# Kernel tuning notes

Hardware: AMD Instinct MI355X
Metric: run time of the kernel (lower is better)

## Reference

```python
import jax, jax.numpy as jnp
import numpy as np

NUM_EMBED = 1024
NUM_HEADS = 16
BLOCK_SIZE = 2048


def setup_inputs() -> dict:
    key = jax.random.key(0)
    k1, k2, k3, k4, k5 = jax.random.split(key, 5)
    C = NUM_EMBED
    s = 1.0 / np.sqrt(C)
    x = jax.random.normal(k1, (2, BLOCK_SIZE, C), dtype=jnp.float32)
    # nn.Linear params: weight (out,in), bias (out,)
    w_attn = jax.random.uniform(k2, (3 * C, C), minval=-s, maxval=s, dtype=jnp.float32)
    b_attn = jax.random.uniform(k3, (3 * C,), minval=-s, maxval=s, dtype=jnp.float32)
    w_proj = jax.random.uniform(k4, (C, C), minval=-s, maxval=s, dtype=jnp.float32)
    b_proj = jax.random.uniform(k5, (C,), minval=-s, maxval=s, dtype=jnp.float32)
    return {"x": x, "w_attn": w_attn, "b_attn": b_attn, "w_proj": w_proj, "b_proj": b_proj}


def reference(x, w_attn, b_attn, w_proj, b_proj):
    B, T, C = x.shape
    H = NUM_HEADS
    D = C // H
    kqv = jnp.einsum('btc,oc->bto', x, w_attn) + b_attn  # (B,T,3C)
    # Original code splits as K, Q, V in that order.
    K, Q, V = jnp.split(kqv, 3, axis=2)
    K = K.reshape(B, T, H, D).transpose(0, 2, 1, 3)  # (B,H,T,D)
    Q = Q.reshape(B, T, H, D).transpose(0, 2, 1, 3)
    V = V.reshape(B, T, H, D).transpose(0, 2, 1, 3)
    aff = jnp.einsum('bhqd,bhkd->bhqk', Q, K) * (D ** -0.5)  # (B,H,T,T)
    causal = jnp.tril(jnp.ones((T, T), dtype=bool))
    aff = jnp.where(causal[None, None], aff, jnp.float32(-jnp.inf))
    wei = jax.nn.softmax(aff, axis=-1)
    attn = jnp.einsum('bhqk,bhkd->bhqd', wei, V)
    attn = attn.transpose(0, 2, 1, 3).reshape(B, T, C)
    out = jnp.einsum('btc,oc->bto', attn, w_proj) + b_proj
    return out
```

## Files before the change

### kernel.cpp

```cpp
#include <hip/hip_runtime.h>
#include <hip/hip_bf16.h>
#include <cstdint>

typedef __attribute__((ext_vector_type(8))) short bf16x8;
typedef __attribute__((ext_vector_type(4))) float f32x4;
typedef __attribute__((ext_vector_type(16))) float f32x16;
typedef __attribute__((ext_vector_type(4))) uint16_t u16x4;

__device__ __forceinline__ uint16_t f2b(float f) {
  union { float f; uint32_t i; } v; v.f = f;
  return (uint16_t)((v.i + 0x7FFFu + ((v.i >> 16) & 1u)) >> 16);
}

__device__ __forceinline__ uint32_t pkbf(float a, float b) {
  union { __hip_bfloat162 h2; uint32_t u; } c;
  c.h2 = __float22bfloat162_rn(make_float2(a, b));
  return c.u;
}

#define GLDS16(g, l) __builtin_amdgcn_global_load_lds( \
    (const __attribute__((address_space(1))) void*)(g), \
    (__attribute__((address_space(3))) void*)(l), 16, 0, 0)

__global__ __launch_bounds__(256) void cvt_all(
    const float* __restrict__ x, const float* __restrict__ wa, const float* __restrict__ wp,
    uint16_t* __restrict__ xb, uint16_t* __restrict__ wab, uint16_t* __restrict__ wpb) {
  const int i = (blockIdx.x * 256 + threadIdx.x) * 4;
  const float* src; uint16_t* dst; int off;
  if (i < 4194304)      { src = x;  dst = xb;  off = i; }
  else if (i < 7340032) { src = wa; dst = wab; off = i - 4194304; }
  else                  { src = wp; dst = wpb; off = i - 7340032; }
  const float4 v = *(const float4*)(src + off);
  u16x4 o;
  o.x = f2b(v.x); o.y = f2b(v.y); o.z = f2b(v.z); o.w = f2b(v.w);
  *(u16x4*)(dst + off) = o;
}

template <int BM, bool OUT_BF16>
__global__ __launch_bounds__(256) void gemm_bt_bias(
    const uint16_t* __restrict__ A, const uint16_t* __restrict__ B,
    const float* __restrict__ bias, void* __restrict__ Cv,
    int M, int N, int K) {
  constexpr int MI = BM / 32;
  constexpr int CA = BM / 16;
  constexpr int CPW = (2 * (CA + 8)) / 4;
  constexpr int CT_PITCH = OUT_BF16 ? 72 : 68;
  constexpr size_t CT_BYTES = (size_t)4 * (BM / 2) * CT_PITCH * (OUT_BF16 ? 2 : 4);
  constexpr size_t ST_BYTES = (size_t)(2 * (BM * 32 + 4096)) * 2;
  constexpr size_t LB = CT_BYTES > ST_BYTES ? CT_BYTES : ST_BYTES;
  __shared__ alignas(16) unsigned char ldsb[LB];
  uint16_t* lds = (uint16_t*)ldsb;
  const int offB0 = BM * 32;
  const int offA1 = BM * 32 + 4096;
  const int offB1 = 2 * BM * 32 + 4096;

  const int tid = threadIdx.x;
  const int wave = tid >> 6, lane = tid & 63;
  const int q4 = lane >> 4, l16 = lane & 15;
  const int wm = wave >> 1, wn = wave & 1;
  const long blockM = (long)blockIdx.y * BM;
  const long blockN = (long)blockIdx.x * 128;

  f32x4 acc[MI][4] = {};

  for (int k0 = 0; k0 < K; k0 += 64) {
#pragma unroll
    for (int c = 0; c < CPW; ++c) {
      const int id = c * 4 + wave;
      const uint16_t* mat; long rowBase; int a, kk, off;
      if (id < CA)               { mat = A; rowBase = blockM; a = id;            kk = k0;      off = 0; }
      else if (id < CA + 8)      { mat = B; rowBase = blockN; a = id - CA;       kk = k0;      off = offB0; }
      else if (id < 2 * CA + 8)  { mat = A; rowBase = blockM; a = id - CA - 8;   kk = k0 + 32; off = offA1; }
      else                       { mat = B; rowBase = blockN; a = id - 2*CA - 8; kk = k0 + 32; off = offB1; }
      const int flat = a * 64 + lane;
      const int row = flat >> 2, seg = flat & 3;
      GLDS16(mat + (rowBase + row) * (long)K + kk + seg * 8, lds + off + a * 512);
    }
    __syncthreads();
#pragma unroll
    for (int h = 0; h < 2; ++h) {
      const uint16_t* Ah = lds + (h ? offA1 : 0);
      const uint16_t* Bh = lds + (h ? offB1 : offB0);
      bf16x8 af[MI], bfr[4];
#pragma unroll
      for (int i = 0; i < MI; ++i)
        af[i] = *(const bf16x8*)&Ah[(wm * (BM / 2) + i * 16 + l16) * 32 + q4 * 8];
#pragma unroll
      for (int j = 0; j < 4; ++j)
        bfr[j] = *(const bf16x8*)&Bh[(wn * 64 + j * 16 + l16) * 32 + q4 * 8];
#pragma unroll
      for (int i = 0; i < MI; ++i)
#pragma unroll
        for (int j = 0; j < 4; ++j)
          acc[i][j] = __builtin_amdgcn_mfma_f32_16x16x32_bf16(af[i], bfr[j], acc[i][j], 0, 0, 0);
    }
    __syncthreads();
  }

  if (OUT_BF16) {
    uint16_t* ct = lds + wave * (BM / 2) * 72;
#pragma unroll
    for (int j = 0; j < 4; ++j) {
      const float bv = bias[blockN + wn * 64 + j * 16 + l16];
#pragma unroll
      for (int i = 0; i < MI; ++i)
#pragma unroll
        for (int r = 0; r < 4; ++r)
          ct[(i * 16 + q4 * 4 + r) * 72 + j * 16 + l16] = f2b(acc[i][j][r] + bv);
    }
    __syncthreads();
    uint16_t* Cb = (uint16_t*)Cv;
#pragma unroll
    for (int st = 0; st < BM / 16; ++st) {
      const int flat = st * 64 + lane;
      const int row = flat >> 3, seg = flat & 7;
      const bf16x8 v = *(const bf16x8*)&ct[row * 72 + seg * 8];
      *(bf16x8*)&Cb[(blockM + wm * (BM / 2) + row) * (long)N + blockN + wn * 64 + seg * 8] = v;
    }
  } else {
    float* ct = (float*)ldsb + wave * (BM / 2) * 68;
#pragma unroll
    for (int j = 0; j < 4; ++j) {
      const float bv = bias[blockN + wn * 64 + j * 16 + l16];
#pragma unroll
      for (int i = 0; i < MI; ++i)
#pragma unroll
        for (int r = 0; r < 4; ++r)
          ct[(i * 16 + q4 * 4 + r) * 68 + j * 16 + l16] = acc[i][j][r] + bv;
    }
    __syncthreads();
    float* Cb = (float*)Cv;
#pragma unroll
    for (int st = 0; st < BM / 8; ++st) {
      const int flat = st * 64 + lane;
      const int row = flat >> 4, seg = flat & 15;
      const f32x4 v = *(const f32x4*)&ct[row * 68 + seg * 4];
      *(f32x4*)&Cb[(blockM + wm * (BM / 2) + row) * (long)N + blockN + wn * 64 + seg * 4] = v;
    }
  }
}

__global__ __launch_bounds__(256, 2) void attn_flash(
    const uint16_t* __restrict__ kqv, uint16_t* __restrict__ attn) {
  constexpr int T = 2048, C = 1024, C3 = 3072;
  __shared__ uint16_t KP[128 * 72];
  __shared__ uint16_t Vt[64 * 136];
  uint32_t* VtW = (uint32_t*)Vt;

  const int tid = threadIdx.x;
  const int wave = tid >> 6, lane = tid & 63;
  const int l32 = lane & 31, hh = lane >> 5;
  const int sidx = blockIdx.x >> 5, bh = blockIdx.x & 31;
  const int b = bh >> 4, h = bh & 15;
  const size_t base = (size_t)b * T * C3;
  const int hD = h * 64;

  const int tr = tid >> 3, kch = tid & 7;
  const float sc = 0.125f * 1.4426950408889634f;

  const int qb = (sidx < 8) ? (15 - sidx) : (sidx - 8);
  const int nkt = qb + 1;
  const int qrow = qb * 128 + wave * 32 + l32;

  bf16x8 qf[4];
#pragma unroll
  for (int m = 0; m < 4; ++m)
    qf[m] = *(const bf16x8*)&kqv[base + (size_t)qrow * C3 + C + hD + m * 16 + hh * 8];

  f32x16 o[2] = {};
  float m_i = -1e30f, l_i = 0.f;

  bf16x8 pk[4], pv0[2], pv1[2];
#pragma unroll
  for (int rr = 0; rr < 4; ++rr)
    pk[rr] = *(const bf16x8*)&kqv[base + (size_t)(rr * 32 + tr) * C3 + hD + kch * 8];
#pragma unroll
  for (int s2 = 0; s2 < 2; ++s2) {
    const size_t g = base + (size_t)(2 * (s2 * 32 + tr)) * C3 + 2 * C + hD + kch * 8;
    pv0[s2] = *(const bf16x8*)&kqv[g];
    pv1[s2] = *(const bf16x8*)&kqv[g + C3];
  }

  for (int kt = 0; kt < nkt; ++kt) {
    __syncthreads();
#pragma unroll
    for (int rr = 0; rr < 4; ++rr)
      *(bf16x8*)&KP[(rr * 32 + tr) * 72 + kch * 8] = pk[rr];
#pragma unroll
    for (int s2 = 0; s2 < 2; ++s2) {
      const int colw = ((s2 * 32 + tr) + 8 * kch) & 63;
      const uint32_t* a0 = (const uint32_t*)&pv0[s2];
      const uint32_t* a1 = (const uint32_t*)&pv1[s2];
#pragma unroll
      for (int i = 0; i < 8; ++i) {
        const uint32_t w = (i & 1)
            ? __builtin_amdgcn_perm(a1[i >> 1], a0[i >> 1], 0x07060302u)
            : __builtin_amdgcn_perm(a1[i >> 1], a0[i >> 1], 0x05040100u);
        VtW[(kch * 8 + i) * 68 + colw] = w;
      }
    }
    __syncthreads();
    if (kt + 1 < nkt) {
      const int kb2 = (kt + 1) * 128;
#pragma unroll
      for (int rr = 0; rr < 4; ++rr)
        pk[rr] = *(const bf16x8*)&kqv[base + (size_t)(kb2 + rr * 32 + tr) * C3 + hD + kch * 8];
#pragma unroll
      for (int s2 = 0; s2 < 2; ++s2) {
        const size_t g = base + (size_t)(kb2 + 2 * (s2 * 32 + tr)) * C3 + 2 * C + hD + kch * 8;
        pv0[s2] = *(const bf16x8*)&kqv[g];
        pv1[s2] = *(const bf16x8*)&kqv[g + C3];
      }
    }

    const int kbmax = (kt == qb) ? wave : 3;

    f32x16 z[4];
#pragma unroll
    for (int kb = 0; kb < 4; ++kb) {
      if (kb <= kbmax) {
        f32x16 zz = {};
#pragma unroll
        for (int m = 0; m < 4; ++m) {
          const bf16x8 kf = *(const bf16x8*)&KP[(kb * 32 + l32) * 72 + m * 16 + hh * 8];
          zz = __builtin_amdgcn_mfma_f32_32x32x16_bf16(kf, qf[m], zz, 0, 0, 0);
        }
        if (kt == qb && kb == wave) {
#pragma unroll
          for (int r = 0; r < 16; ++r) {
            const int keyl = (r & 3) + 8 * (r >> 2) + 4 * hh;
            if (keyl > l32) zz[r] = -1e30f;
          }
        }
        z[kb] = zz;
      }
    }

    float mloc = -1e30f;
#pragma unroll
    for (int kb = 0; kb < 4; ++kb)
      if (kb <= kbmax)
#pragma unroll
        for (int r = 0; r < 16; ++r) mloc = fmaxf(mloc, z[kb][r]);
    mloc = fmaxf(mloc, __shfl_xor(mloc, 32, 64));
    const float mnew = fmaxf(m_i, mloc * sc);
    const float alpha = exp2f(m_i - mnew);
    const bool mchg = mnew > m_i;
    m_i = mnew;
    float rs = 0.f;
#pragma unroll
    for (int kb = 0; kb < 4; ++kb)
      if (kb <= kbmax)
#pragma unroll
        for (int r = 0; r < 16; ++r) {
          const float pe = exp2f(fmaf(z[kb][r], sc, -mnew));
          z[kb][r] = pe;
          rs += pe;
        }
    rs += __shfl_xor(rs, 32, 64);
    l_i = l_i * alpha + rs;
    if (__any(mchg)) {
#pragma unroll
      for (int r = 0; r < 16; ++r) {
        const float ar = __shfl(alpha, (r & 3) + 8 * (r >> 2) + 4 * hh, 64);
        o[0][r] *= ar;
        o[1][r] *= ar;
      }
    }

#pragma unroll
    for (int kb = 0; kb < 4; ++kb) {
      if (kb <= kbmax) {
        uint32_t x0 = pkbf(z[kb][0], z[kb][1]),   x1 = pkbf(z[kb][2], z[kb][3]);
        uint32_t y0 = pkbf(z[kb][4], z[kb][5]),   y1 = pkbf(z[kb][6], z[kb][7]);
        uint32_t x2 = pkbf(z[kb][8], z[kb][9]),   x3 = pkbf(z[kb][10], z[kb][11]);
        uint32_t y2 = pkbf(z[kb][12], z[kb][13]), y3 = pkbf(z[kb][14], z[kb][15]);
        const uint32_t s0 = hh ? x0 : y0, s1 = hh ? x1 : y1;
        const uint32_t s2 = hh ? x2 : y2, s3 = hh ? x3 : y3;
        const uint32_t t0 = __shfl_xor(s0, 32, 64), t1 = __shfl_xor(s1, 32, 64);
        const uint32_t t2 = __shfl_xor(s2, 32, 64), t3 = __shfl_xor(s3, 32, 64);
#pragma unroll
        for (int cc = 0; cc < 2; ++cc) {
          const int c = 2 * kb + cc;
          union { bf16x8 v; uint32_t w[4]; } pa;
          if (cc == 0) {
            pa.w[0] = hh ? t0 : x0; pa.w[1] = hh ? t1 : x1;
            pa.w[2] = hh ? y0 : t0; pa.w[3] = hh ? y1 : t1;
          } else {
            pa.w[0] = hh ? t2 : x2; pa.w[1] = hh ? t3 : x3;
            pa.w[2] = hh ? y2 : t2; pa.w[3] = hh ? y3 : t3;
          }
#pragma unroll
          for (int db = 0; db < 2; ++db) {
            const int d = db * 32 + l32;
            const int col = (c * 16 + hh * 8 + 16 * (d >> 3)) & 127;
            const bf16x8 vf = *(const bf16x8*)&Vt[d * 136 + col];
            o[db] = __builtin_amdgcn_mfma_f32_32x32x16_bf16(pa.v, vf, o[db], 0, 0, 0);
          }
        }
      }
    }
  }

  const size_t obase = (size_t)b * T * C;
  const float linv = 1.0f / l_i;
#pragma unroll
  for (int r = 0; r < 16; ++r) {
    const int ql = (r & 3) + 8 * (r >> 2) + 4 * hh;
    const float lr = __shfl(linv, ql, 64);
    const int q = qb * 128 + wave * 32 + ql;
    const size_t rowoff = obase + (size_t)q * C + hD;
    attn[rowoff + l32] = f2b(o[0][r] * lr);
    attn[rowoff + 32 + l32] = f2b(o[1][r] * lr);
  }
}

extern "C" void kernel_launch(void* const* d_in, const int* in_sizes, int n_in,
                              void* d_out, int out_size, void* d_ws, size_t ws_size,
                              hipStream_t stream) {
  const float* x      = (const float*)d_in[0];
  const float* w_attn = (const float*)d_in[1];
  const float* b_attn = (const float*)d_in[2];
  const float* w_proj = (const float*)d_in[3];
  const float* b_proj = (const float*)d_in[4];
  float* out = (float*)d_out;

  uint16_t* xb    = (uint16_t*)d_ws;
  uint16_t* wab   = xb  + (size_t)4096 * 1024;
  uint16_t* wpb   = wab + (size_t)3072 * 1024;
  uint16_t* kqv   = wpb + (size_t)1024 * 1024;
  uint16_t* attnb = kqv + (size_t)4096 * 3072;

  dim3 blk(256, 1, 1);
  hipLaunchKernelGGL(cvt_all, dim3(8192), blk, 0, stream, x, w_attn, w_proj, xb, wab, wpb);

  hipLaunchKernelGGL((gemm_bt_bias<128, true>), dim3(3072 / 128, 4096 / 128, 1), blk, 0, stream,
                     xb, wab, b_attn, (void*)kqv, 4096, 3072, 1024);
  hipLaunchKernelGGL(attn_flash, dim3(512, 1, 1), blk, 0, stream, kqv, attnb);
  hipLaunchKernelGGL((gemm_bt_bias<64, false>), dim3(1024 / 128, 4096 / 64, 1), blk, 0, stream,
                     attnb, wpb, b_proj, (void*)out, 4096, 1024, 1024);
}
```

Measured before the change: 201.1 us.

## Split long causal query blocks across two KV chunks with a merge pass

New measurement: 236.8 us. +17.7%, slower.

```diff
diff --git a/kernel.cpp b/kernel.cpp
--- a/kernel.cpp
+++ b/kernel.cpp
@@ -140,8 +140,9 @@
   }
 }
 
-__global__ __launch_bounds__(256, 2) void attn_flash(
-    const uint16_t* __restrict__ kqv, uint16_t* __restrict__ attn) {
+__global__ __launch_bounds__(256, 3) void attn_part(
+    const uint16_t* __restrict__ kqv, uint16_t* __restrict__ attn,
+    float* __restrict__ pO, float* __restrict__ pml) {
   constexpr int T = 2048, C = 1024, C3 = 3072;
   __shared__ uint16_t KP[128 * 72];
   __shared__ uint16_t Vt[64 * 136];
@@ -150,16 +151,29 @@
   const int tid = threadIdx.x;
   const int wave = tid >> 6, lane = tid & 63;
   const int l32 = lane & 31, hh = lane >> 5;
-  const int sidx = blockIdx.x >> 5, bh = blockIdx.x & 31;
+  const int g = blockIdx.x >> 8;
+  const int rs = blockIdx.x & 255;
+  const int s = rs & 7, bh = rs >> 3;
   const int b = bh >> 4, h = bh & 15;
   const size_t base = (size_t)b * T * C3;
   const int hD = h * 64;
 
+  static const unsigned char QBT[24] = {15,14, 7,13,13,12, 6,10,
+                                        15,14,12,11,11,10, 9, 5,
+                                         0, 1, 2, 3, 8, 9, 8, 4};
+  static const unsigned char CHT[24] = { 0, 0, 2, 0, 1, 0, 2, 0,
+                                         1, 1, 1, 0, 1, 1, 1, 2,
+                                         2, 2, 2, 2, 1, 0, 0, 2};
+  const int idx = g * 8 + s;
+  const int qb = QBT[idx], ch = CHT[idx];
+  const int hsp = (qb + 2) >> 1;
+  const bool sp = (ch != 2);
+  const int kt0 = (ch == 1) ? hsp : 0;
+  const int kt1 = (ch == 0) ? hsp : qb + 1;
+
   const int tr = tid >> 3, kch = tid & 7;
   const float sc = 0.125f * 1.4426950408889634f;
 
-  const int qb = (sidx < 8) ? (15 - sidx) : (sidx - 8);
-  const int nkt = qb + 1;
   const int qrow = qb * 128 + wave * 32 + l32;
 
   bf16x8 qf[4];
@@ -171,17 +185,20 @@
   float m_i = -1e30f, l_i = 0.f;
 
   bf16x8 pk[4], pv0[2], pv1[2];
-#pragma unroll
-  for (int rr = 0; rr < 4; ++rr)
-    pk[rr] = *(const bf16x8*)&kqv[base + (size_t)(rr * 32 + tr) * C3 + hD + kch * 8];
-#pragma unroll
-  for (int s2 = 0; s2 < 2; ++s2) {
-    const size_t g = base + (size_t)(2 * (s2 * 32 + tr)) * C3 + 2 * C + hD + kch * 8;
-    pv0[s2] = *(const bf16x8*)&kqv[g];
-    pv1[s2] = *(const bf16x8*)&kqv[g + C3];
+  {
+    const int kA = kt0 * 128;
+#pragma unroll
+    for (int rr = 0; rr < 4; ++rr)
+      pk[rr] = *(const bf16x8*)&kqv[base + (size_t)(kA + rr * 32 + tr) * C3 + hD + kch * 8];
+#pragma unroll
+    for (int s2 = 0; s2 < 2; ++s2) {
+      const size_t gg = base + (size_t)(kA + 2 * (s2 * 32 + tr)) * C3 + 2 * C + hD + kch * 8;
+      pv0[s2] = *(const bf16x8*)&kqv[gg];
+      pv1[s2] = *(const bf16x8*)&kqv[gg + C3];
+    }
   }
 
-  for (int kt = 0; kt < nkt; ++kt) {
+  for (int kt = kt0; kt < kt1; ++kt) {
     __syncthreads();
 #pragma unroll
     for (int rr = 0; rr < 4; ++rr)
@@ -200,16 +217,16 @@
       }
     }
     __syncthreads();
-    if (kt + 1 < nkt) {
+    if (kt + 1 < kt1) {
       const int kb2 = (kt + 1) * 128;
 #pragma unroll
       for (int rr = 0; rr < 4; ++rr)
         pk[rr] = *(const bf16x8*)&kqv[base + (size_t)(kb2 + rr * 32 + tr) * C3 + hD + kch * 8];
 #pragma unroll
       for (int s2 = 0; s2 < 2; ++s2) {
-        const size_t g = base + (size_t)(kb2 + 2 * (s2 * 32 + tr)) * C3 + 2 * C + hD + kch * 8;
-        pv0[s2] = *(const bf16x8*)&kqv[g];
-        pv1[s2] = *(const bf16x8*)&kqv[g + C3];
+        const size_t gg = base + (size_t)(kb2 + 2 * (s2 * 32 + tr)) * C3 + 2 * C + hD + kch * 8;
+        pv0[s2] = *(const bf16x8*)&kqv[gg];
+        pv1[s2] = *(const bf16x8*)&kqv[gg + C3];
       }
     }
 
@@ -247,7 +264,7 @@
     const float alpha = exp2f(m_i - mnew);
     const bool mchg = mnew > m_i;
     m_i = mnew;
-    float rs = 0.f;
+    float rs2 = 0.f;
 #pragma unroll
     for (int kb = 0; kb < 4; ++kb)
       if (kb <= kbmax)
@@ -255,10 +272,10 @@
         for (int r = 0; r < 16; ++r) {
           const float pe = exp2f(fmaf(z[kb][r], sc, -mnew));
           z[kb][r] = pe;
-          rs += pe;
+          rs2 += pe;
         }
-    rs += __shfl_xor(rs, 32, 64);
-    l_i = l_i * alpha + rs;
+    rs2 += __shfl_xor(rs2, 32, 64);
+    l_i = l_i * alpha + rs2;
     if (__any(mchg)) {
 #pragma unroll
       for (int r = 0; r < 16; ++r) {
@@ -302,17 +319,60 @@
     }
   }
 
-  const size_t obase = (size_t)b * T * C;
-  const float linv = 1.0f / l_i;
-#pragma unroll
-  for (int r = 0; r < 16; ++r) {
-    const int ql = (r & 3) + 8 * (r >> 2) + 4 * hh;
-    const float lr = __shfl(linv, ql, 64);
-    const int q = qb * 128 + wave * 32 + ql;
-    const size_t rowoff = obase + (size_t)q * C + hD;
-    attn[rowoff + l32] = f2b(o[0][r] * lr);
-    attn[rowoff + 32 + l32] = f2b(o[1][r] * lr);
+  if (!sp) {
+    const size_t obase = (size_t)b * T * C;
+    const float linv = 1.0f / l_i;
+#pragma unroll
+    for (int r = 0; r < 16; ++r) {
+      const int ql = (r & 3) + 8 * (r >> 2) + 4 * hh;
+      const float lr = __shfl(linv, ql, 64);
+      const int q = qb * 128 + wave * 32 + ql;
+      const size_t rowoff = obase + (size_t)q * C + hD;
+      attn[rowoff + l32] = f2b(o[0][r] * lr);
+      attn[rowoff + 32 + l32] = f2b(o[1][r] * lr);
+    }
+  } else {
+    const int slot = (bh * 8 + (qb - 8)) * 2 + ch;
+    float* po = pO + (size_t)slot * 8192;
+#pragma unroll
+    for (int r = 0; r < 16; ++r) {
+      const int ql = (r & 3) + 8 * (r >> 2) + 4 * hh;
+      const int row = wave * 32 + ql;
+      po[row * 64 + l32] = o[0][r];
+      po[row * 64 + 32 + l32] = o[1][r];
+    }
+    if (hh == 0) {
+      pml[slot * 256 + wave * 32 + l32] = m_i;
+      pml[slot * 256 + 128 + wave * 32 + l32] = l_i;
+    }
   }
+}
+
+__global__ __launch_bounds__(256) void attn_merge(
+    const float* __restrict__ pO, const float* __restrict__ pml,
+    uint16_t* __restrict__ attn) {
+  constexpr int T = 2048, C = 1024;
+  const int tid = threadIdx.x;
+  const int gid = blockIdx.x * 8 + (tid >> 5);
+  const int l32 = tid & 31;
+  const int pair = gid >> 7, q = gid & 127;
+  const int bh = pair >> 3, qb = (pair & 7) + 8;
+  const int b = bh >> 4, h = bh & 15;
+  const int slot0 = pair * 2, slot1 = slot0 + 1;
+
+  const float m0 = pml[slot0 * 256 + q], l0 = pml[slot0 * 256 + 128 + q];
+  const float m1 = pml[slot1 * 256 + q], l1 = pml[slot1 * 256 + 128 + q];
+  const float M = fmaxf(m0, m1);
+  const float w0 = exp2f(m0 - M), w1 = exp2f(m1 - M);
+  const float dn = 1.0f / (l0 * w0 + l1 * w1);
+
+  const float2 a = *(const float2*)(pO + (size_t)slot0 * 8192 + q * 64 + l32 * 2);
+  const float2 c = *(const float2*)(pO + (size_t)slot1 * 8192 + q * 64 + l32 * 2);
+  const float o0 = (a.x * w0 + c.x * w1) * dn;
+  const float o1 = (a.y * w0 + c.y * w1) * dn;
+
+  const size_t off = ((size_t)b * T + qb * 128 + q) * C + h * 64 + l32 * 2;
+  *(uint32_t*)&attn[off] = pkbf(o0, o1);
 }
 
 extern "C" void kernel_launch(void* const* d_in, const int* in_sizes, int n_in,
@@ -331,12 +391,16 @@
   uint16_t* kqv   = wpb + (size_t)1024 * 1024;
   uint16_t* attnb = kqv + (size_t)4096 * 3072;
 
+  float* pO  = (float*)d_out;
+  float* pml = (float*)xb;
+
   dim3 blk(256, 1, 1);
   hipLaunchKernelGGL(cvt_all, dim3(8192), blk, 0, stream, x, w_attn, w_proj, xb, wab, wpb);
 
   hipLaunchKernelGGL((gemm_bt_bias<128, true>), dim3(3072 / 128, 4096 / 128, 1), blk, 0, stream,
                      xb, wab, b_attn, (void*)kqv, 4096, 3072, 1024);
-  hipLaunchKernelGGL(attn_flash, dim3(512, 1, 1), blk, 0, stream, kqv, attnb);
+  hipLaunchKernelGGL(attn_part, dim3(768, 1, 1), blk, 0, stream, kqv, attnb, pO, pml);
+  hipLaunchKernelGGL(attn_merge, dim3(4096, 1, 1), blk, 0, stream, pO, pml, attnb);
   hipLaunchKernelGGL((gemm_bt_bias<64, false>), dim3(1024 / 128, 4096 / 64, 1), blk, 0, stream,
                      attnb, wpb, b_proj, (void*)out, 4096, 1024, 1024);
 }
```

## Split attention keys across waves with 64-query blocks and LDS softmax merge

Applied to the files above, without the earlier changes.

New measurement: 191.2 us. -4.9%, faster.

```diff
diff --git a/kernel.cpp b/kernel.cpp
--- a/kernel.cpp
+++ b/kernel.cpp
@@ -143,9 +143,12 @@
 __global__ __launch_bounds__(256, 2) void attn_flash(
     const uint16_t* __restrict__ kqv, uint16_t* __restrict__ attn) {
   constexpr int T = 2048, C = 1024, C3 = 3072;
-  __shared__ uint16_t KP[128 * 72];
-  __shared__ uint16_t Vt[64 * 136];
-  uint32_t* VtW = (uint32_t*)Vt;
+  __shared__ alignas(16) unsigned char ldsb[35840];
+  uint16_t* KP = (uint16_t*)ldsb;
+  uint16_t* Vt = (uint16_t*)(ldsb + 18432);
+  uint32_t* VtW = (uint32_t*)(ldsb + 18432);
+  float* mlb  = (float*)ldsb;
+  float* obuf = (float*)(ldsb + 1024);
 
   const int tid = threadIdx.x;
   const int wave = tid >> 6, lane = tid & 63;
@@ -154,21 +157,20 @@
   const int b = bh >> 4, h = bh & 15;
   const size_t base = (size_t)b * T * C3;
   const int hD = h * 64;
-
+  const int qb = 31 - sidx;
+  const int nkt = (qb >> 1) + 1;
   const int tr = tid >> 3, kch = tid & 7;
   const float sc = 0.125f * 1.4426950408889634f;
 
-  const int qb = (sidx < 8) ? (15 - sidx) : (sidx - 8);
-  const int nkt = qb + 1;
-  const int qrow = qb * 128 + wave * 32 + l32;
-
-  bf16x8 qf[4];
-#pragma unroll
-  for (int m = 0; m < 4; ++m)
-    qf[m] = *(const bf16x8*)&kqv[base + (size_t)qrow * C3 + C + hD + m * 16 + hh * 8];
-
-  f32x16 o[2] = {};
-  float m_i = -1e30f, l_i = 0.f;
+  bf16x8 qf[2][4];
+#pragma unroll
+  for (int qc = 0; qc < 2; ++qc)
+#pragma unroll
+    for (int m = 0; m < 4; ++m)
+      qf[qc][m] = *(const bf16x8*)&kqv[base + (size_t)(qb * 64 + qc * 32 + l32) * C3 + C + hD + m * 16 + hh * 8];
+
+  f32x16 o[2][2] = {};
+  float m_i[2] = {-1e30f, -1e30f}, l_i[2] = {0.f, 0.f};
 
   bf16x8 pk[4], pv0[2], pv1[2];
 #pragma unroll
@@ -176,9 +178,9 @@
     pk[rr] = *(const bf16x8*)&kqv[base + (size_t)(rr * 32 + tr) * C3 + hD + kch * 8];
 #pragma unroll
   for (int s2 = 0; s2 < 2; ++s2) {
-    const size_t g = base + (size_t)(2 * (s2 * 32 + tr)) * C3 + 2 * C + hD + kch * 8;
-    pv0[s2] = *(const bf16x8*)&kqv[g];
-    pv1[s2] = *(const bf16x8*)&kqv[g + C3];
+    const size_t gg = base + (size_t)(2 * (s2 * 32 + tr)) * C3 + 2 * C + hD + kch * 8;
+    pv0[s2] = *(const bf16x8*)&kqv[gg];
+    pv1[s2] = *(const bf16x8*)&kqv[gg + C3];
   }
 
   for (int kt = 0; kt < nkt; ++kt) {
@@ -207,81 +209,71 @@
         pk[rr] = *(const bf16x8*)&kqv[base + (size_t)(kb2 + rr * 32 + tr) * C3 + hD + kch * 8];
 #pragma unroll
       for (int s2 = 0; s2 < 2; ++s2) {
-        const size_t g = base + (size_t)(kb2 + 2 * (s2 * 32 + tr)) * C3 + 2 * C + hD + kch * 8;
-        pv0[s2] = *(const bf16x8*)&kqv[g];
-        pv1[s2] = *(const bf16x8*)&kqv[g + C3];
+        const size_t gg = base + (size_t)(kb2 + 2 * (s2 * 32 + tr)) * C3 + 2 * C + hD + kch * 8;
+        pv0[s2] = *(const bf16x8*)&kqv[gg];
+        pv1[s2] = *(const bf16x8*)&kqv[gg + C3];
       }
     }
 
-    const int kbmax = (kt == qb) ? wave : 3;
-
-    f32x16 z[4];
-#pragma unroll
-    for (int kb = 0; kb < 4; ++kb) {
-      if (kb <= kbmax) {
-        f32x16 zz = {};
-#pragma unroll
-        for (int m = 0; m < 4; ++m) {
-          const bf16x8 kf = *(const bf16x8*)&KP[(kb * 32 + l32) * 72 + m * 16 + hh * 8];
-          zz = __builtin_amdgcn_mfma_f32_32x32x16_bf16(kf, qf[m], zz, 0, 0, 0);
-        }
-        if (kt == qb && kb == wave) {
+    const bool act = (kt * 128 + wave * 32) <= (qb * 64 + 63);
+    if (act) {
+      bf16x8 kf[4];
+#pragma unroll
+      for (int m = 0; m < 4; ++m)
+        kf[m] = *(const bf16x8*)&KP[(wave * 32 + l32) * 72 + m * 16 + hh * 8];
+
+#pragma unroll
+      for (int qc = 0; qc < 2; ++qc) {
+        f32x16 z = {};
+#pragma unroll
+        for (int m = 0; m < 4; ++m)
+          z = __builtin_amdgcn_mfma_f32_32x32x16_bf16(kf[m], qf[qc][m], z, 0, 0, 0);
+        if (kt == nkt - 1) {
+          const int key0 = kt * 128 + wave * 32;
+          const int qg = qb * 64 + qc * 32 + l32;
 #pragma unroll
           for (int r = 0; r < 16; ++r) {
-            const int keyl = (r & 3) + 8 * (r >> 2) + 4 * hh;
-            if (keyl > l32) zz[r] = -1e30f;
+            const int kg = key0 + (r & 3) + 8 * (r >> 2) + 4 * hh;
+            if (kg > qg) z[r] = -1e30f;
           }
         }
-        z[kb] = zz;
-      }
-    }
-
-    float mloc = -1e30f;
-#pragma unroll
-    for (int kb = 0; kb < 4; ++kb)
-      if (kb <= kbmax)
-#pragma unroll
-        for (int r = 0; r < 16; ++r) mloc = fmaxf(mloc, z[kb][r]);
-    mloc = fmaxf(mloc, __shfl_xor(mloc, 32, 64));
-    const float mnew = fmaxf(m_i, mloc * sc);
-    const float alpha = exp2f(m_i - mnew);
-    const bool mchg = mnew > m_i;
-    m_i = mnew;
-    float rs = 0.f;
-#pragma unroll
-    for (int kb = 0; kb < 4; ++kb)
-      if (kb <= kbmax)
+        float mloc = -1e30f;
+#pragma unroll
+        for (int r = 0; r < 16; ++r) mloc = fmaxf(mloc, z[r]);
+        mloc = fmaxf(mloc, __shfl_xor(mloc, 32, 64));
+        const float pm = fmaxf(mloc * sc, -3.0e4f);
+        if (__any(pm - m_i[qc] > 8.0f)) {
+          const float mnew = fmaxf(m_i[qc], pm);
+          const float alpha = exp2f(m_i[qc] - mnew);
+#pragma unroll
+          for (int r = 0; r < 16; ++r) {
+            const float ar = __shfl(alpha, (r & 3) + 8 * (r >> 2) + 4 * hh, 64);
+            o[qc][0][r] *= ar;
+            o[qc][1][r] *= ar;
+          }
+          l_i[qc] *= alpha;
+          m_i[qc] = mnew;
+        }
+        float rs = 0.f;
 #pragma unroll
         for (int r = 0; r < 16; ++r) {
-          const float pe = exp2f(fmaf(z[kb][r], sc, -mnew));
-          z[kb][r] = pe;
+          const float pe = exp2f(fmaf(z[r], sc, -m_i[qc]));
+          z[r] = pe;
           rs += pe;
         }
-    rs += __shfl_xor(rs, 32, 64);
-    l_i = l_i * alpha + rs;
-    if (__any(mchg)) {
-#pragma unroll
-      for (int r = 0; r < 16; ++r) {
-        const float ar = __shfl(alpha, (r & 3) + 8 * (r >> 2) + 4 * hh, 64);
-        o[0][r] *= ar;
-        o[1][r] *= ar;
-      }
-    }
-
-#pragma unroll
-    for (int kb = 0; kb < 4; ++kb) {
-      if (kb <= kbmax) {
-        uint32_t x0 = pkbf(z[kb][0], z[kb][1]),   x1 = pkbf(z[kb][2], z[kb][3]);
-        uint32_t y0 = pkbf(z[kb][4], z[kb][5]),   y1 = pkbf(z[kb][6], z[kb][7]);
-        uint32_t x2 = pkbf(z[kb][8], z[kb][9]),   x3 = pkbf(z[kb][10], z[kb][11]);
-        uint32_t y2 = pkbf(z[kb][12], z[kb][13]), y3 = pkbf(z[kb][14], z[kb][15]);
+        rs += __shfl_xor(rs, 32, 64);
+        l_i[qc] += rs;
+
+        uint32_t x0 = pkbf(z[0], z[1]),   x1 = pkbf(z[2], z[3]);
+        uint32_t y0 = pkbf(z[4], z[5]),   y1 = pkbf(z[6], z[7]);
+        uint32_t x2 = pkbf(z[8], z[9]),   x3 = pkbf(z[10], z[11]);
+        uint32_t y2 = pkbf(z[12], z[13]), y3 = pkbf(z[14], z[15]);
         const uint32_t s0 = hh ? x0 : y0, s1 = hh ? x1 : y1;
         const uint32_t s2 = hh ? x2 : y2, s3 = hh ? x3 : y3;
         const uint32_t t0 = __shfl_xor(s0, 32, 64), t1 = __shfl_xor(s1, 32, 64);
         const uint32_t t2 = __shfl_xor(s2, 32, 64), t3 = __shfl_xor(s3, 32, 64);
 #pragma unroll
         for (int cc = 0; cc < 2; ++cc) {
-          const int c = 2 * kb + cc;
           union { bf16x8 v; uint32_t w[4]; } pa;
           if (cc == 0) {
             pa.w[0] = hh ? t0 : x0; pa.w[1] = hh ? t1 : x1;
@@ -293,25 +285,56 @@
 #pragma unroll
           for (int db = 0; db < 2; ++db) {
             const int d = db * 32 + l32;
-            const int col = (c * 16 + hh * 8 + 16 * (d >> 3)) & 127;
+            const int col = (wave * 32 + cc * 16 + hh * 8 + 16 * (d >> 3)) & 127;
             const bf16x8 vf = *(const bf16x8*)&Vt[d * 136 + col];
-            o[db] = __builtin_amdgcn_mfma_f32_32x32x16_bf16(pa.v, vf, o[db], 0, 0, 0);
+            o[qc][db] = __builtin_amdgcn_mfma_f32_32x32x16_bf16(pa.v, vf, o[qc][db], 0, 0, 0);
           }
         }
       }
     }
   }
 
-  const size_t obase = (size_t)b * T * C;
-  const float linv = 1.0f / l_i;
-#pragma unroll
-  for (int r = 0; r < 16; ++r) {
-    const int ql = (r & 3) + 8 * (r >> 2) + 4 * hh;
-    const float lr = __shfl(linv, ql, 64);
-    const int q = qb * 128 + wave * 32 + ql;
-    const size_t rowoff = obase + (size_t)q * C + hD;
-    attn[rowoff + l32] = f2b(o[0][r] * lr);
-    attn[rowoff + 32 + l32] = f2b(o[1][r] * lr);
+#pragma unroll
+  for (int qc = 0; qc < 2; ++qc) {
+    __syncthreads();
+    if (hh == 0) {
+      mlb[wave * 64 + l32] = m_i[qc];
+      mlb[wave * 64 + 32 + l32] = l_i[qc];
+    }
+#pragma unroll
+    for (int r = 0; r < 16; ++r) {
+      const int ql = (r & 3) + 8 * (r >> 2) + 4 * hh;
+      const int bw = wave * 2112 + ql * 66 + l32;
+      obuf[bw] = o[qc][0][r];
+      obuf[bw + 32] = o[qc][1][r];
+    }
+    __syncthreads();
+    float mw[4], lw[4];
+#pragma unroll
+    for (int w = 0; w < 4; ++w) {
+      mw[w] = mlb[w * 64 + l32];
+      lw[w] = mlb[w * 64 + 32 + l32];
+    }
+    const float M = fmaxf(fmaxf(mw[0], mw[1]), fmaxf(mw[2], mw[3]));
+    float L = 0.f, ww[4];
+#pragma unroll
+    for (int w = 0; w < 4; ++w) { ww[w] = exp2f(mw[w] - M); L += lw[w] * ww[w]; }
+    const float Li = 1.0f / L;
+    const int cb = wave * 2 + hh;
+    float acc[8] = {};
+#pragma unroll
+    for (int w = 0; w < 4; ++w)
+#pragma unroll
+      for (int p = 0; p < 4; ++p) {
+        const float2 v = *(const float2*)&obuf[w * 2112 + l32 * 66 + cb * 8 + p * 2];
+        acc[2 * p]     += v.x * ww[w];
+        acc[2 * p + 1] += v.y * ww[w];
+      }
+    union { bf16x8 v; uint32_t w4[4]; } ov;
+#pragma unroll
+    for (int p = 0; p < 4; ++p)
+      ov.w4[p] = pkbf(acc[2 * p] * Li, acc[2 * p + 1] * Li);
+    *(bf16x8*)&attn[((size_t)b * T + qb * 64 + qc * 32 + l32) * C + hD + cb * 8] = ov.v;
   }
 }
 
@@ -336,7 +359,7 @@
 
   hipLaunchKernelGGL((gemm_bt_bias<128, true>), dim3(3072 / 128, 4096 / 128, 1), blk, 0, stream,
                      xb, wab, b_attn, (void*)kqv, 4096, 3072, 1024);
-  hipLaunchKernelGGL(attn_flash, dim3(512, 1, 1), blk, 0, stream, kqv, attnb);
+  hipLaunchKernelGGL(attn_flash, dim3(1024, 1, 1), blk, 0, stream, kqv, attnb);
   hipLaunchKernelGGL((gemm_bt_bias<64, false>), dim3(1024 / 128, 4096 / 64, 1), blk, 0, stream,
                      attnb, wpb, b_proj, (void*)out, 4096, 1024, 1024);
 }
```
